# Performance work log

Hardware: AMD Instinct MI355X
Metric: run time of the kernel (lower is better)

The kernel has to match this reference:

```python
import jax, jax.numpy as jnp
import numpy as np

K = 512
H = 8
B = 8
T = 1024
EPS = 1e-5


def _layernorm(x, g, b):
    mu = jnp.mean(x, axis=-1, keepdims=True)
    var = jnp.var(x, axis=-1, keepdims=True)
    return (x - mu) * jax.lax.rsqrt(var + EPS) * g + b


def _attention(x, enc, wq, wk, wv, wo):
    b, t, k = x.shape
    h = H
    scale = k ** (-0.25)
    q = (x @ wq).reshape(b, t, h, k) * scale        # [b,t,h,k]
    kk = (enc @ wk).reshape(b, t, h, k) * scale
    v = (enc @ wv).reshape(b, t, h, k)
    dot = jnp.einsum('bqhd,bkhd->bhqk', q, kk)      # [b,h,t,t]
    att = jax.nn.softmax(dot, axis=-1)
    out = jnp.einsum('bhqk,bkhd->bqhd', att, v).reshape(b, t, h * k)
    return out @ wo                                  # [b,t,k]


def setup_inputs() -> dict:
    key = jax.random.key(0)
    ks = jax.random.split(key, 12)
    s = 0.02
    return {
        'x': jax.random.normal(ks[0], (B, T, K), jnp.float32),
        'enc': jax.random.normal(ks[1], (B, T, K), jnp.float32),
        'sa_wq': jax.random.normal(ks[2], (K, K * H), jnp.float32) * s,
        'sa_wk': jax.random.normal(ks[3], (K, K * H), jnp.float32) * s,
        'sa_wv': jax.random.normal(ks[4], (K, K * H), jnp.float32) * s,
        'sa_wo': jax.random.normal(ks[5], (K * H, K), jnp.float32) * s,
        'ca_wq': jax.random.normal(ks[6], (K, K * H), jnp.float32) * s,
        'ca_wk': jax.random.normal(ks[7], (K, K * H), jnp.float32) * s,
        'ca_wv': jax.random.normal(ks[8], (K, K * H), jnp.float32) * s,
        'ca_wo': jax.random.normal(ks[9], (K * H, K), jnp.float32) * s,
        'ln1_g': jnp.ones((K,), jnp.float32), 'ln1_b': jnp.zeros((K,), jnp.float32),
        'ln2_g': jnp.ones((K,), jnp.float32), 'ln2_b': jnp.zeros((K,), jnp.float32),
        'ln3_g': jnp.ones((K,), jnp.float32), 'ln3_b': jnp.zeros((K,), jnp.float32),
        'ff_w1': jax.random.normal(ks[10], (K, 4 * K), jnp.float32) * s,
        'ff_b1': jnp.zeros((4 * K,), jnp.float32),
        'ff_w2': jax.random.normal(ks[11], (4 * K, K), jnp.float32) * s,
        'ff_b2': jnp.zeros((K,), jnp.float32),
    }


def reference(x, enc, sa_wq, sa_wk, sa_wv, sa_wo, ca_wq, ca_wk, ca_wv, ca_wo,
              ln1_g, ln1_b, ln2_g, ln2_b, ln3_g, ln3_b,
              ff_w1, ff_b1, ff_w2, ff_b2):
    # masked self-attention (mask_future_steps=False -> plain self-attn)
    sa = _attention(x, x, sa_wq, sa_wk, sa_wv, sa_wo)
    x = _layernorm(sa + x, ln1_g, ln1_b)
    # encoder-decoder attention
    ca = _attention(x, enc, ca_wq, ca_wk, ca_wv, ca_wo)
    x = _layernorm(ca + x, ln2_g, ln2_b)
    # dropout p=0.0 -> identity
    ff = jax.nn.relu(x @ ff_w1 + ff_b1) @ ff_w2 + ff_b2
    x = _layernorm(ff + x, ln3_g, ln3_b)
    return x
```

## Files before the change

kernel.cpp:

```cpp
#include <hip/hip_runtime.h>
#include <stdint.h>

typedef short short8 __attribute__((ext_vector_type(8)));
typedef float f32x4 __attribute__((ext_vector_type(4)));

#define DEVI static __device__ __forceinline__

DEVI float b2f(unsigned short u) {
  union { float f; uint32_t i; } v; v.i = ((uint32_t)u) << 16; return v.f;
}
DEVI unsigned short f2b(float f) {
  union { float f; uint32_t i; } v; v.f = f;
  uint32_t r = v.i + 0x7FFFu + ((v.i >> 16) & 1u);
  return (unsigned short)(r >> 16);
}

DEVI void async_cp16(const unsigned short* g, unsigned short* l) {
  __builtin_amdgcn_global_load_lds(
      (const __attribute__((address_space(1))) void*)g,
      (__attribute__((address_space(3))) void*)l, 16, 0, 0);
}

DEVI void swz(int& bx, int& by, int& bz) {
  const int gx = gridDim.x, gy = gridDim.y, gz = gridDim.z;
  int l = blockIdx.x + gx * (blockIdx.y + gy * blockIdx.z);
  bz = l % gz; l /= gz;
  by = l % gy;
  bx = l / gy;
}


__global__ __launch_bounds__(256) void cvt_f32_bf16(
    const float4* __restrict__ src, unsigned short* __restrict__ dst) {
  const int i = blockIdx.x * 256 + threadIdx.x;
  float4 f = src[i];
  uint2 o;
  o.x = (uint32_t)f2b(f.x) | ((uint32_t)f2b(f.y) << 16);
  o.y = (uint32_t)f2b(f.z) | ((uint32_t)f2b(f.w) << 16);
  ((uint2*)dst)[i] = o;
}

__global__ __launch_bounds__(256) void wtrans(
    const float* __restrict__ src, unsigned short* __restrict__ dst, int R, int C) {
  __shared__ float tile[32][33];
  const int tx = threadIdx.x & 31, ty = threadIdx.x >> 5;
  const int c0 = blockIdx.x * 32, r0 = blockIdx.y * 32;
#pragma unroll
  for (int i = 0; i < 32; i += 8)
    tile[ty + i][tx] = src[(long)(r0 + ty + i) * C + c0 + tx];
  __syncthreads();
#pragma unroll
  for (int i = 0; i < 32; i += 8)
    dst[(long)(c0 + ty + i) * R + r0 + tx] = f2b(tile[tx][ty + i]);
}

__global__ __launch_bounds__(256) void softmax_rows(
    unsigned short* __restrict__ S, int NZ) {
  const int tid = threadIdx.x;
  const int bx = blockIdx.x;
  const long z = bx % NZ, r = bx / NZ;
  unsigned short* p = S + (z * 1024 + r) * 1024;
  float v[4];
  float m = -3.0e38f;
#pragma unroll
  for (int i = 0; i < 4; i++) { v[i] = b2f(p[tid + 256 * i]); m = fmaxf(m, v[i]); }
#pragma unroll
  for (int o = 1; o < 64; o <<= 1) m = fmaxf(m, __shfl_xor(m, o));
  __shared__ float rm[4], rsum[4];
  const int lane = tid & 63, wave = tid >> 6;
  if (lane == 0) rm[wave] = m;
  __syncthreads();
  m = fmaxf(fmaxf(rm[0], rm[1]), fmaxf(rm[2], rm[3]));
  float s = 0.f;
#pragma unroll
  for (int i = 0; i < 4; i++) { v[i] = __expf(v[i] - m); s += v[i]; }
#pragma unroll
  for (int o = 1; o < 64; o <<= 1) s += __shfl_xor(s, o);
  if (lane == 0) rsum[wave] = s;
  __syncthreads();
  s = rsum[0] + rsum[1] + rsum[2] + rsum[3];
  const float inv = 1.f / s;
#pragma unroll
  for (int i = 0; i < 4; i++) p[tid + 256 * i] = f2b(v[i] * inv);
}

__global__ __launch_bounds__(256) void layernorm_rows(
    const float* X, const float* __restrict__ g,
    const float* __restrict__ b, float* Y,
    unsigned short* __restrict__ Yb) {
  const int tid = threadIdx.x;
  const long row = blockIdx.x;
  const float* x = X + row * 512;
  float v0 = x[tid], v1 = x[tid + 256];
  float s1 = v0 + v1;
  float s2 = v0 * v0 + v1 * v1;
#pragma unroll
  for (int o = 1; o < 64; o <<= 1) {
    s1 += __shfl_xor(s1, o);
    s2 += __shfl_xor(s2, o);
  }
  __shared__ float r1[4], r2[4];
  const int lane = tid & 63, wave = tid >> 6;
  if (lane == 0) { r1[wave] = s1; r2[wave] = s2; }
  __syncthreads();
  s1 = r1[0] + r1[1] + r1[2] + r1[3];
  s2 = r2[0] + r2[1] + r2[2] + r2[3];
  const float mu = s1 * (1.f / 512.f);
  const float var = s2 * (1.f / 512.f) - mu * mu;
  const float rs = rsqrtf(var + 1e-5f);
  float y0 = (v0 - mu) * rs * g[tid] + b[tid];
  float y1 = (v1 - mu) * rs * g[tid + 256] + b[tid + 256];
  if (Y) { Y[row * 512 + tid] = y0; Y[row * 512 + tid + 256] = y1; }
  if (Yb) { Yb[row * 512 + tid] = f2b(y0); Yb[row * 512 + tid + 256] = f2b(y1); }
}

template <int EPI>
__global__ __launch_bounds__(256, 2) void gemm_bt(
    const unsigned short* __restrict__ A, int lda, long asb, long ash,
    const unsigned short* __restrict__ B, int ldb, long bsb, long bsh,
    void* Cv, int ldc, long csb, long csh,
    int K, float scale,
    const float* __restrict__ bias, const float* res) {
  __shared__ __align__(16) unsigned short As[128 * 32];
  __shared__ __align__(16) unsigned short Bs[128 * 32];
  int bx, by, bz;
  swz(bx, by, bz);
  const int tid = threadIdx.x;
  const int lane = tid & 63;
  const int wave = tid >> 6;
  const int zb = bz >> 3, zh = bz & 7;
  const int m0 = by * 128;
  const int n0 = bx * 128;

  const unsigned short* Ab = A + zb * asb + zh * ash + (long)m0 * lda;
  const unsigned short* Bb = B + zb * bsb + zh * bsh + (long)n0 * ldb;

  const int r0 = tid >> 2;
  const int p0 = (tid & 3) << 3;

  f32x4 acc[4][4];
#pragma unroll
  for (int i = 0; i < 4; i++)
#pragma unroll
    for (int j = 0; j < 4; j++) acc[i][j] = (f32x4){0.f, 0.f, 0.f, 0.f};

  const int wm = (wave >> 1) << 6;
  const int wn = (wave & 1) << 6;
  const int fm = lane & 15;
  const int k8 = (lane >> 4) << 3;

  for (int kt = 0; kt < K; kt += 32) {
    __syncthreads();
    async_cp16(Ab + (long)r0 * lda + kt + p0, &As[tid * 8]);
    async_cp16(Ab + (long)(r0 + 64) * lda + kt + p0, &As[2048 + tid * 8]);
    async_cp16(Bb + (long)r0 * ldb + kt + p0, &Bs[tid * 8]);
    async_cp16(Bb + (long)(r0 + 64) * ldb + kt + p0, &Bs[2048 + tid * 8]);
    __syncthreads();

    short8 af[4], bfr[4];
#pragma unroll
    for (int i = 0; i < 4; i++)
      af[i] = *(const short8*)&As[(wm + i * 16 + fm) * 32 + k8];
#pragma unroll
    for (int j = 0; j < 4; j++)
      bfr[j] = *(const short8*)&Bs[(wn + j * 16 + fm) * 32 + k8];
#pragma unroll
    for (int i = 0; i < 4; i++)
#pragma unroll
      for (int j = 0; j < 4; j++)
        acc[i][j] = __builtin_amdgcn_mfma_f32_16x16x32_bf16(af[i], bfr[j], acc[i][j], 0, 0, 0);
  }

  const long coff = zb * csb + zh * csh;
  const int er = (lane >> 4) << 2;
  const int ec = lane & 15;
#pragma unroll
  for (int i = 0; i < 4; i++) {
#pragma unroll
    for (int j = 0; j < 4; j++) {
      const int gc = n0 + wn + j * 16 + ec;
#pragma unroll
      for (int r = 0; r < 4; r++) {
        const int gr = m0 + wm + i * 16 + er + r;
        const float v = acc[i][j][r];
        const long idx = coff + (long)gr * ldc + gc;
        if constexpr (EPI == 0) {
          ((unsigned short*)Cv)[idx] = f2b(v * scale);
        } else if constexpr (EPI == 1) {
          float o = v;
          if (bias) o += bias[gc];
          if (res) o += res[(long)gr * ldc + gc];
          ((float*)Cv)[idx] = o;
        } else {
          ((unsigned short*)Cv)[idx] = f2b(fmaxf(v + bias[gc], 0.f));
        }
      }
    }
  }
}

extern "C" void kernel_launch(void* const* d_in, const int* in_sizes, int n_in,
                              void* d_out, int out_size, void* d_ws, size_t ws_size,
                              hipStream_t stream) {
  const float* x     = (const float*)d_in[0];
  const float* enc   = (const float*)d_in[1];
  const float* ln1_g = (const float*)d_in[10];
  const float* ln1_b = (const float*)d_in[11];
  const float* ln2_g = (const float*)d_in[12];
  const float* ln2_b = (const float*)d_in[13];
  const float* ln3_g = (const float*)d_in[14];
  const float* ln3_b = (const float*)d_in[15];
  const float* ff_b1 = (const float*)d_in[17];
  const float* ff_b2 = (const float*)d_in[19];

  uint8_t* ws = (uint8_t*)d_ws;
  auto US = [&](size_t o) { return (unsigned short*)(ws + o); };
  auto F  = [&](size_t o) { return (float*)(ws + o); };

  const size_t MB = 1ull << 20;
  const size_t SZ_WBIG = 4 * MB, SZ_WFF = 2 * MB;

  const size_t O_XB = 0, O_ENCB = 8 * MB, O_WT = 16 * MB;
  const size_t O_RES = 52 * MB;
  const size_t O_XNB = 68 * MB;
  auto WT = [&](int i) { return US(O_WT + (size_t)i * SZ_WBIG); };

  int HP = 1;
  for (int c = 8; c >= 1; c >>= 1)
    if (ws_size >= (76 + 40 * (size_t)c) * MB) { HP = c; break; }
  const int NG = 8 / HP;
  const int NZ = HP * 8;
  const int LD = HP * 512;
  const size_t O_QG  = 76 * MB;
  const size_t O_KG  = O_QG + (size_t)HP * 8 * MB;
  const size_t O_VTG = O_KG + (size_t)HP * 8 * MB;
  const size_t O_SG  = O_VTG + (size_t)HP * 8 * MB;
  const size_t O_H   = 76 * MB;

  const float qsc = 0.21022410381342863f;
  dim3 B256(256);

  cvt_f32_bf16<<<4096, B256, 0, stream>>>((const float4*)x, US(O_XB));
  cvt_f32_bf16<<<4096, B256, 0, stream>>>((const float4*)enc, US(O_ENCB));

  struct WSpec { const float* s; size_t off; int R, C; };
  const WSpec wspec[10] = {
      {(const float*)d_in[2], O_WT + 0 * SZ_WBIG, 512, 4096},
      {(const float*)d_in[3], O_WT + 1 * SZ_WBIG, 512, 4096},
      {(const float*)d_in[4], O_WT + 2 * SZ_WBIG, 512, 4096},
      {(const float*)d_in[5], O_WT + 3 * SZ_WBIG, 4096, 512},
      {(const float*)d_in[6], O_WT + 4 * SZ_WBIG, 512, 4096},
      {(const float*)d_in[7], O_WT + 5 * SZ_WBIG, 512, 4096},
      {(const float*)d_in[8], O_WT + 6 * SZ_WBIG, 512, 4096},
      {(const float*)d_in[9], O_WT + 7 * SZ_WBIG, 4096, 512},
      {(const float*)d_in[16], O_WT + 8 * SZ_WBIG, 512, 2048},
      {(const float*)d_in[18], O_WT + 8 * SZ_WBIG + SZ_WFF, 2048, 512},
  };
  for (int i = 0; i < 10; i++)
    wtrans<<<dim3(wspec[i].C / 32, wspec[i].R / 32), B256, 0, stream>>>(
        wspec[i].s, US(wspec[i].off), wspec[i].R, wspec[i].C);

  auto attention = [&](const unsigned short* qsrc, const unsigned short* kvsrc,
                       int wb, const float* resid) {
    for (int g = 0; g < NG; g++) {
      const size_t woff = (size_t)g * LD * 512;
      gemm_bt<0><<<dim3(HP * 4, 64, 1), B256, 0, stream>>>(
          qsrc, 512, 0, 0, WT(wb + 0) + woff, 512, 0, 0,
          US(O_QG), LD, 0, 0, 512, qsc, nullptr, nullptr);
      gemm_bt<0><<<dim3(HP * 4, 64, 1), B256, 0, stream>>>(
          kvsrc, 512, 0, 0, WT(wb + 1) + woff, 512, 0, 0,
          US(O_KG), LD, 0, 0, 512, qsc, nullptr, nullptr);
      gemm_bt<0><<<dim3(64, HP * 4, 1), B256, 0, stream>>>(
          WT(wb + 2) + woff, 512, 0, 0, kvsrc, 512, 0, 0,
          US(O_VTG), 8192, 0, 0, 512, 1.f, nullptr, nullptr);
      gemm_bt<0><<<dim3(8, 8, NZ), B256, 0, stream>>>(
          US(O_QG), LD, 512L, (long)1024 * LD,
          US(O_KG), LD, 512L, (long)1024 * LD,
          US(O_SG), 1024, 8388608L, 1048576L, 512, 1.f, nullptr, nullptr);
      softmax_rows<<<NZ * 1024, B256, 0, stream>>>(US(O_SG), NZ);
      gemm_bt<0><<<dim3(4, 8, NZ), B256, 0, stream>>>(
          US(O_SG), 1024, 8388608L, 1048576L,
          US(O_VTG), 8192, 4194304L, 1024L,
          US(O_QG), LD, 512L, (long)1024 * LD, 1024, 1.f, nullptr, nullptr);
      gemm_bt<1><<<dim3(4, 64, 1), B256, 0, stream>>>(
          US(O_QG), LD, 0, 0, WT(wb + 3) + (size_t)g * LD, 4096, 0, 0,
          F(O_RES), 512, 0, 0, LD, 1.f, nullptr, g == 0 ? resid : F(O_RES));
    }
  };

  attention(US(O_XB), US(O_XB), 0, x);
  layernorm_rows<<<8192, B256, 0, stream>>>(F(O_RES), ln1_g, ln1_b, F(O_RES), US(O_XNB));
  attention(US(O_XNB), US(O_ENCB), 4, F(O_RES));
  layernorm_rows<<<8192, B256, 0, stream>>>(F(O_RES), ln2_g, ln2_b, F(O_RES), US(O_XNB));
  gemm_bt<2><<<dim3(16, 64, 1), B256, 0, stream>>>(
      US(O_XNB), 512, 0, 0, WT(8), 512, 0, 0,
      US(O_H), 2048, 0, 0, 512, 1.f, ff_b1, nullptr);
  gemm_bt<1><<<dim3(4, 64, 1), B256, 0, stream>>>(
      US(O_H), 2048, 0, 0, US(O_WT + 8 * SZ_WBIG + SZ_WFF), 2048, 0, 0,
      F(O_RES), 512, 0, 0, 2048, 1.f, ff_b2, F(O_RES));
  layernorm_rows<<<8192, B256, 0, stream>>>(F(O_RES), ln3_g, ln3_b, (float*)d_out, nullptr);
}
```

Before: 1.351 ms.

## Add 64x64 GEMM kernel and process attention one head at a time

Adds a smaller 64x64-tile MFMA GEMM kernel with a single LDS buffer and uses it for all attention GEMMs and the second FFN GEMM. The attention loop now always runs one head per iteration with batch as the grid z dimension, replacing the workspace-size-dependent head-grouping. This raises block count and occupancy for the small per-head GEMMs. In exchange it loses the larger-tile data reuse, issues more kernel launches than when several heads were grouped, and the new kernel has no load/compute overlap.

Result: slower. 1.876 ms (+38.9%).

```diff
diff --git a/kernel.cpp b/kernel.cpp
--- a/kernel.cpp
+++ b/kernel.cpp
@@ -189,7 +189,90 @@
         } else if constexpr (EPI == 1) {
           float o = v;
           if (bias) o += bias[gc];
-          if (res) o += res[(long)gr * ldc + gc];
+          if (res) o += res[idx];
+          ((float*)Cv)[idx] = o;
+        } else {
+          ((unsigned short*)Cv)[idx] = f2b(fmaxf(v + bias[gc], 0.f));
+        }
+      }
+    }
+  }
+}
+
+template <int EPI>
+__global__ __launch_bounds__(256) void gemm64(
+    const unsigned short* __restrict__ A, int lda, long asb, long ash,
+    const unsigned short* __restrict__ B, int ldb, long bsb, long bsh,
+    void* Cv, int ldc, long csb, long csh,
+    int K, float scale,
+    const float* __restrict__ bias, const float* res) {
+  __shared__ __align__(16) unsigned short As[64 * 32];
+  __shared__ __align__(16) unsigned short Bs[64 * 32];
+  int bx, by, bz;
+  swz(bx, by, bz);
+  const int tid = threadIdx.x;
+  const int lane = tid & 63;
+  const int wave = tid >> 6;
+  const int zb = bz >> 3, zh = bz & 7;
+  const int m0 = by * 64;
+  const int n0 = bx * 64;
+
+  const unsigned short* Ab = A + zb * asb + zh * ash + (long)m0 * lda;
+  const unsigned short* Bb = B + zb * bsb + zh * bsh + (long)n0 * ldb;
+
+  const int r0 = tid >> 2;
+  const int p0 = (tid & 3) << 3;
+
+  f32x4 acc[2][2];
+#pragma unroll
+  for (int i = 0; i < 2; i++)
+#pragma unroll
+    for (int j = 0; j < 2; j++) acc[i][j] = (f32x4){0.f, 0.f, 0.f, 0.f};
+
+  const int wm = (wave >> 1) << 5;
+  const int wn = (wave & 1) << 5;
+  const int fm = lane & 15;
+  const int k8 = (lane >> 4) << 3;
+
+  for (int kt = 0; kt < K; kt += 32) {
+    __syncthreads();
+    async_cp16(Ab + (long)r0 * lda + kt + p0, &As[tid * 8]);
+    async_cp16(Bb + (long)r0 * ldb + kt + p0, &Bs[tid * 8]);
+    __syncthreads();
+
+    short8 af[2], bfr[2];
+#pragma unroll
+    for (int i = 0; i < 2; i++)
+      af[i] = *(const short8*)&As[(wm + i * 16 + fm) * 32 + k8];
+#pragma unroll
+    for (int j = 0; j < 2; j++)
+      bfr[j] = *(const short8*)&Bs[(wn + j * 16 + fm) * 32 + k8];
+#pragma unroll
+    for (int i = 0; i < 2; i++)
+#pragma unroll
+      for (int j = 0; j < 2; j++)
+        acc[i][j] = __builtin_amdgcn_mfma_f32_16x16x32_bf16(af[i], bfr[j], acc[i][j], 0, 0, 0);
+  }
+
+  const long coff = zb * csb + zh * csh;
+  const int er = (lane >> 4) << 2;
+  const int ec = lane & 15;
+#pragma unroll
+  for (int i = 0; i < 2; i++) {
+#pragma unroll
+    for (int j = 0; j < 2; j++) {
+      const int gc = n0 + wn + j * 16 + ec;
+#pragma unroll
+      for (int r = 0; r < 4; r++) {
+        const int gr = m0 + wm + i * 16 + er + r;
+        const float v = acc[i][j][r];
+        const long idx = coff + (long)gr * ldc + gc;
+        if constexpr (EPI == 0) {
+          ((unsigned short*)Cv)[idx] = f2b(v * scale);
+        } else if constexpr (EPI == 1) {
+          float o = v;
+          if (bias) o += bias[gc];
+          if (res) o += res[idx];
           ((float*)Cv)[idx] = o;
         } else {
           ((unsigned short*)Cv)[idx] = f2b(fmaxf(v + bias[gc], 0.f));
@@ -223,22 +306,14 @@
   const size_t O_XB = 0, O_ENCB = 8 * MB, O_WT = 16 * MB;
   const size_t O_RES = 52 * MB;
   const size_t O_XNB = 68 * MB;
+  const size_t O_QG = 76 * MB, O_KG = 84 * MB, O_VTG = 92 * MB, O_SG = 100 * MB;
+  const size_t O_H  = 76 * MB;
   auto WT = [&](int i) { return US(O_WT + (size_t)i * SZ_WBIG); };
-
-  int HP = 1;
-  for (int c = 8; c >= 1; c >>= 1)
-    if (ws_size >= (76 + 40 * (size_t)c) * MB) { HP = c; break; }
-  const int NG = 8 / HP;
-  const int NZ = HP * 8;
-  const int LD = HP * 512;
-  const size_t O_QG  = 76 * MB;
-  const size_t O_KG  = O_QG + (size_t)HP * 8 * MB;
-  const size_t O_VTG = O_KG + (size_t)HP * 8 * MB;
-  const size_t O_SG  = O_VTG + (size_t)HP * 8 * MB;
-  const size_t O_H   = 76 * MB;
 
   const float qsc = 0.21022410381342863f;
   dim3 B256(256);
+  const long RB = 524288L;
+  const long SB = 1048576L;
 
   cvt_f32_bf16<<<4096, B256, 0, stream>>>((const float4*)x, US(O_XB));
   cvt_f32_bf16<<<4096, B256, 0, stream>>>((const float4*)enc, US(O_ENCB));
@@ -262,29 +337,27 @@
 
   auto attention = [&](const unsigned short* qsrc, const unsigned short* kvsrc,
                        int wb, const float* resid) {
-    for (int g = 0; g < NG; g++) {
-      const size_t woff = (size_t)g * LD * 512;
-      gemm_bt<0><<<dim3(HP * 4, 64, 1), B256, 0, stream>>>(
-          qsrc, 512, 0, 0, WT(wb + 0) + woff, 512, 0, 0,
-          US(O_QG), LD, 0, 0, 512, qsc, nullptr, nullptr);
-      gemm_bt<0><<<dim3(HP * 4, 64, 1), B256, 0, stream>>>(
-          kvsrc, 512, 0, 0, WT(wb + 1) + woff, 512, 0, 0,
-          US(O_KG), LD, 0, 0, 512, qsc, nullptr, nullptr);
-      gemm_bt<0><<<dim3(64, HP * 4, 1), B256, 0, stream>>>(
-          WT(wb + 2) + woff, 512, 0, 0, kvsrc, 512, 0, 0,
-          US(O_VTG), 8192, 0, 0, 512, 1.f, nullptr, nullptr);
-      gemm_bt<0><<<dim3(8, 8, NZ), B256, 0, stream>>>(
-          US(O_QG), LD, 512L, (long)1024 * LD,
-          US(O_KG), LD, 512L, (long)1024 * LD,
-          US(O_SG), 1024, 8388608L, 1048576L, 512, 1.f, nullptr, nullptr);
-      softmax_rows<<<NZ * 1024, B256, 0, stream>>>(US(O_SG), NZ);
-      gemm_bt<0><<<dim3(4, 8, NZ), B256, 0, stream>>>(
-          US(O_SG), 1024, 8388608L, 1048576L,
-          US(O_VTG), 8192, 4194304L, 1024L,
-          US(O_QG), LD, 512L, (long)1024 * LD, 1024, 1.f, nullptr, nullptr);
-      gemm_bt<1><<<dim3(4, 64, 1), B256, 0, stream>>>(
-          US(O_QG), LD, 0, 0, WT(wb + 3) + (size_t)g * LD, 4096, 0, 0,
-          F(O_RES), 512, 0, 0, LD, 1.f, nullptr, g == 0 ? resid : F(O_RES));
+    for (int h = 0; h < 8; h++) {
+      const size_t woff = (size_t)h * 512 * 512;
+      gemm64<0><<<dim3(8, 16, 8), B256, 0, stream>>>(
+          qsrc, 512, 0, RB, WT(wb + 0) + woff, 512, 0, 0,
+          US(O_QG), 512, 0, RB, 512, qsc, nullptr, nullptr);
+      gemm64<0><<<dim3(8, 16, 8), B256, 0, stream>>>(
+          kvsrc, 512, 0, RB, WT(wb + 1) + woff, 512, 0, 0,
+          US(O_KG), 512, 0, RB, 512, qsc, nullptr, nullptr);
+      gemm64<0><<<dim3(16, 8, 8), B256, 0, stream>>>(
+          WT(wb + 2) + woff, 512, 0, 0, kvsrc, 512, 0, RB,
+          US(O_VTG), 8192, 0, 1024L, 512, 1.f, nullptr, nullptr);
+      gemm64<0><<<dim3(16, 16, 8), B256, 0, stream>>>(
+          US(O_QG), 512, 0, RB, US(O_KG), 512, 0, RB,
+          US(O_SG), 1024, 0, SB, 512, 1.f, nullptr, nullptr);
+      softmax_rows<<<8192, B256, 0, stream>>>(US(O_SG), 8);
+      gemm64<0><<<dim3(8, 16, 8), B256, 0, stream>>>(
+          US(O_SG), 1024, 0, SB, US(O_VTG), 8192, 0, 1024L,
+          US(O_QG), 512, 0, RB, 1024, 1.f, nullptr, nullptr);
+      gemm64<1><<<dim3(8, 16, 8), B256, 0, stream>>>(
+          US(O_QG), 512, 0, RB, WT(wb + 3) + (size_t)h * 512, 4096, 0, 0,
+          F(O_RES), 512, 0, RB, 512, 1.f, nullptr, h == 0 ? resid : F(O_RES));
     }
   };
 
@@ -295,7 +368,7 @@
   gemm_bt<2><<<dim3(16, 64, 1), B256, 0, stream>>>(
       US(O_XNB), 512, 0, 0, WT(8), 512, 0, 0,
       US(O_H), 2048, 0, 0, 512, 1.f, ff_b1, nullptr);
-  gemm_bt<1><<<dim3(4, 64, 1), B256, 0, stream>>>(
+  gemm64<1><<<dim3(8, 128, 1), B256, 0, stream>>>(
       US(O_H), 2048, 0, 0, US(O_WT + 8 * SZ_WBIG + SZ_WFF), 2048, 0, 0,
       F(O_RES), 512, 0, 0, 2048, 1.f, ff_b2, F(O_RES));
   layernorm_rows<<<8192, B256, 0, stream>>>(F(O_RES), ln3_g, ln3_b, (float*)d_out, nullptr);
```
